# Optimization experiments

Measured on AMD Instinct MI355X. Metric: run time of the kernel, lower is better.

Reference implementation:

```python
import jax, jax.numpy as jnp
import numpy as np
import math

D_MODEL = 1024
EPS = 1e-6  # RMSNorm epsilon


def setup_inputs() -> dict:
    key = jax.random.key(0)
    ks = jax.random.split(key, 9)
    d = D_MODEL
    B, T = 4, 4096
    s = 1.0 / math.sqrt(d)
    return {
        "x": jax.random.normal(ks[0], (B, T, d), dtype=jnp.float32),
        "w_key": jax.random.normal(ks[1], (2 * d, d), dtype=jnp.float32) * s,  # Linear(d, 2d, bias=False)
        "conv_w": jax.random.normal(ks[2], (d, 1, 3), dtype=jnp.float32) * (1.0 / math.sqrt(3)),  # depthwise k=3
        "conv_b": jax.random.normal(ks[3], (d,), dtype=jnp.float32) * 0.02,
        "w1": jax.random.normal(ks[4], (2 * d, d), dtype=jnp.float32) * s,  # Linear(d, 2d)
        "b1": jax.random.normal(ks[5], (2 * d,), dtype=jnp.float32) * 0.02,
        "w2": jax.random.normal(ks[6], (d, 2 * d), dtype=jnp.float32) * (1.0 / math.sqrt(2 * d)),  # Linear(2d, d)
        "b2": jax.random.normal(ks[7], (d,), dtype=jnp.float32) * 0.02,
        "norm_w": jnp.ones((d,), dtype=jnp.float32),
    }


def parallel_lerp_scan(theta, alpha):
    # h_t = lerp(h_{t-1}, theta_t, alpha_t) = (1-alpha_t)*h_{t-1} + alpha_t*theta_t
    # Linear recurrence h_t = a_t*h_{t-1} + b_t -> log-depth associative scan.
    a = 1.0 - alpha
    b = alpha * theta

    def combine(c1, c2):
        a1, b1 = c1
        a2, b2 = c2
        return (a2 * a1, a2 * b1 + b2)

    _, h = jax.lax.associative_scan(combine, (a, b), axis=1)
    return h


def rms_norm(x, w):
    var = jnp.mean(jnp.square(x), axis=-1, keepdims=True)
    return x * jax.lax.rsqrt(var + EPS) * w


def reference(x, w_key, conv_w, conv_b, w1, b1, w2, b2, norm_w):
    d = x.shape[-1]
    res = jnp.einsum('btd,ed->bte', x, w_key)  # [B,T,2D]
    theta, alpha = res[..., :d], res[..., d:]
    h = parallel_lerp_scan(jnp.tanh(theta) * math.pi, jax.nn.sigmoid(alpha))
    h = h.astype(x.dtype)
    # causal depthwise conv: left-pad (k-1)=2 zeros along time
    h_t = jnp.transpose(h, (0, 2, 1))  # [B,D,T]
    conv = jax.lax.conv_general_dilated(
        h_t, conv_w, window_strides=(1,), padding=[(2, 0)],
        feature_group_count=d, dimension_numbers=('NCH', 'OIH', 'NCH'))
    h_bound = jnp.transpose(conv + conv_b[None, :, None], (0, 2, 1))  # [B,T,D]
    z = h + h_bound
    hid = jax.nn.silu(jnp.einsum('btd,ed->bte', z, w1) + b1)
    h_final = jnp.einsum('bte,de->btd', hid, w2) + b2
    return rms_norm(h_final, norm_w)
```

## Files before the change

### kernel.cpp

```cpp
#include <hip/hip_runtime.h>

typedef unsigned short u16;
typedef unsigned int u32;
typedef __attribute__((ext_vector_type(8))) short short8;
typedef __attribute__((ext_vector_type(4))) float f32x4;

#define T_LEN 4096
#define BATCH 4
#define M_TOT (BATCH*T_LEN)
#define NCHUNK 32
#define CLEN 128

__device__ __forceinline__ u16 f2bf(float f){
  u32 u = __builtin_bit_cast(u32, f);
  u32 r = (u + 0x7FFFu + ((u >> 16) & 1u)) >> 16;
  return (u16)r;
}
__device__ __forceinline__ float bf2f(u16 h){
  u32 u = ((u32)h) << 16; return __builtin_bit_cast(float, u);
}
__device__ __forceinline__ float sigmoid_(float v){ return 1.f/(1.f + __expf(-v)); }
__device__ __forceinline__ float tanh_pi_(float v){
  return 3.14159265358979323846f * (1.f - 2.f/(1.f + __expf(2.f*v)));
}

__global__ __launch_bounds__(256) void cvt_bf16_k(const float* __restrict__ in,
                                                  u16* __restrict__ out, int n4){
  int g = blockIdx.x*256 + threadIdx.x;
  if (g >= n4) return;
  float4 v = reinterpret_cast<const float4*>(in)[g];
  reinterpret_cast<ushort4*>(out)[g] =
      make_ushort4(f2bf(v.x), f2bf(v.y), f2bf(v.z), f2bf(v.w));
}

#define BAR() __builtin_amdgcn_s_barrier()
#define VMCNT(n) asm volatile("s_waitcnt vmcnt(" #n ")" ::: "memory")
#define PRIO1() __builtin_amdgcn_s_setprio(1)
#define PRIO0() __builtin_amdgcn_s_setprio(0)
#define SGBPIN(R) do { __builtin_amdgcn_sched_group_barrier(0x100, R, 0); \
                       __builtin_amdgcn_sched_group_barrier(0x008, 16, 0); } while(0)

#define STAGE(buf, ab, q, kt) do { \
  const u16* _s = ((ab) ? Bb : Ab) + (size_t)(q)*rowK64 + (size_t)(kt)*64; \
  __builtin_amdgcn_global_load_lds( \
    (const __attribute__((address_space(1))) void*)_s, \
    (__attribute__((address_space(3))) void*)(smem + (buf)*65536 + (ab)*32768 + (q)*8192 + stb), \
    16, 0, 0); \
} while(0)

#define LDA(buf, m, kk) (*(const short8*)(smem + (buf)*65536 + aRow + (m)*2048 + ((kk) ? csw1 : csw0)))
#define LDB(buf, n, kk) (*(const short8*)(smem + (buf)*65536 + 32768 + bRow + (n)*2048 + ((kk) ? csw1 : csw0)))

#define PFA(dst, buf, q) do { \
  dst[0] = LDA(buf, 2*(q),   0); \
  dst[1] = LDA(buf, 2*(q),   1); \
  dst[2] = LDA(buf, 2*(q)+1, 0); \
  dst[3] = LDA(buf, 2*(q)+1, 1); } while(0)

#define PFBH(d0, d1, buf, half) do { \
  d0[2*(half)]   = LDB(buf, 2*(half),   0); \
  d1[2*(half)]   = LDB(buf, 2*(half),   1); \
  d0[2*(half)+1] = LDB(buf, 2*(half)+1, 0); \
  d1[2*(half)+1] = LDB(buf, 2*(half)+1, 1); } while(0)

#define PFB(d0, d1, buf) do { PFBH(d0,d1,buf,0); PFBH(d0,d1,buf,1); } while(0)

#define MFMA_Q(q, A, B0, B1) do { _Pragma("unroll") \
  for (int n=0;n<4;n++){ \
    acc[2*(q)][n]   = __builtin_amdgcn_mfma_f32_16x16x32_bf16(A[0], B0[n], acc[2*(q)][n], 0,0,0); \
    acc[2*(q)][n]   = __builtin_amdgcn_mfma_f32_16x16x32_bf16(A[1], B1[n], acc[2*(q)][n], 0,0,0); \
    acc[2*(q)+1][n] = __builtin_amdgcn_mfma_f32_16x16x32_bf16(A[2], B0[n], acc[2*(q)+1][n], 0,0,0); \
    acc[2*(q)+1][n] = __builtin_amdgcn_mfma_f32_16x16x32_bf16(A[3], B1[n], acc[2*(q)+1][n], 0,0,0); \
  } } while(0)

template<int EPI>
__global__ __launch_bounds__(512, 2) void gemm8p(
    const u16* __restrict__ Ag, const u16* __restrict__ Bg,
    const float* __restrict__ bias, void* __restrict__ Cout,
    int M, int N, int K)
{
  extern __shared__ __attribute__((aligned(16))) char smem[];
  const int tid = threadIdx.x;
  const int wid = tid >> 6, lane = tid & 63;
  const int wr = wid >> 2, wc = wid & 3;
  const int fr = lane & 15, fq = lane >> 4;

  const int nbn = N >> 8;
  const int nwg = gridDim.x;
  const int bid = blockIdx.x;
  const int swzb = (bid & 7) * (nwg >> 3) + (bid >> 3);
  const int bm = swzb / nbn, bn = swzb - bm * nbn;

  const size_t rowK64 = (size_t)64 * K;
  const u16* Ab = Ag + ((size_t)bm*256 + (tid>>3)) * K + ((tid & 7) ^ ((tid >> 3) & 7)) * 8;
  const u16* Bb = Bg + ((size_t)bn*256 + (tid>>3)) * K + ((tid & 7) ^ ((tid >> 3) & 7)) * 8;
  const u32 stb = (u32)(wid << 10);

  const u32 aRow = (u32)(wr*128 + fr) * 128;
  const u32 bRow = (u32)(wc*64  + fr) * 128;
  const u32 csw0 = (u32)((fq*16)      ^ ((fr & 7) << 4));
  const u32 csw1 = (u32)((64 + fq*16) ^ ((fr & 7) << 4));

  f32x4 acc[8][4];
#pragma unroll
  for (int m=0;m<8;m++)
#pragma unroll
    for (int n=0;n<4;n++) acc[m][n] = f32x4{0.f,0.f,0.f,0.f};

  short8 bP0[4], bP1[4], bN0[4], bN1[4];
  short8 aP[4], aN[4];

  const int NT = K >> 6;

  STAGE(0,1,0,0); STAGE(0,1,1,0); STAGE(0,1,2,0); STAGE(0,1,3,0);
  STAGE(0,0,0,0); STAGE(0,0,1,0); STAGE(0,0,2,0); STAGE(0,0,3,0);
  STAGE(1,1,0,1); STAGE(1,1,1,1); STAGE(1,1,2,1); STAGE(1,1,3,1);
  STAGE(1,0,0,1); STAGE(1,0,2,1);
  VMCNT(6);
  BAR();
  PFB(bP0, bP1, 0);
  PFA(aP, 0, 0);

  for (int i = 0; i < (NT>>1) - 1; ++i){
    const int tt = 2*i;
    STAGE(1,0,1,tt+1); STAGE(1,0,3,tt+1);
    BAR();
    PRIO1(); PFA(aN,0,1); MFMA_Q(0, aP, bP0, bP1); PRIO0(); SGBPIN(4);
    BAR();
    STAGE(0,1,0,tt+2); STAGE(0,1,1,tt+2);
    BAR();
    PRIO1(); PFA(aP,0,2); MFMA_Q(1, aN, bP0, bP1); PRIO0(); SGBPIN(4);
    BAR();
    STAGE(0,1,2,tt+2); STAGE(0,1,3,tt+2);
    BAR();
    PRIO1(); PFA(aN,0,3); MFMA_Q(2, aP, bP0, bP1); PRIO0(); SGBPIN(4);
    BAR();
    STAGE(0,0,0,tt+2); STAGE(0,0,2,tt+2);
    BAR();
    VMCNT(6);
    PRIO1(); PFA(aP,1,0); PFBH(bN0,bN1,1,0); MFMA_Q(3, aN, bP0, bP1); PRIO0(); SGBPIN(8);
    BAR();
    STAGE(0,0,1,tt+2); STAGE(0,0,3,tt+2);
    BAR();
    PRIO1(); PFBH(bN0,bN1,1,1); PFA(aN,1,1); MFMA_Q(0, aP, bN0, bN1); PRIO0(); SGBPIN(8);
    BAR();
    STAGE(1,1,0,tt+3); STAGE(1,1,1,tt+3);
    BAR();
    PRIO1(); PFA(aP,1,2); MFMA_Q(1, aN, bN0, bN1); PRIO0(); SGBPIN(4);
    BAR();
    STAGE(1,1,2,tt+3); STAGE(1,1,3,tt+3);
    BAR();
    VMCNT(8);
    PRIO1(); PFA(aN,1,3); PFBH(bP0,bP1,0,0); MFMA_Q(2, aP, bN0, bN1); PRIO0(); SGBPIN(8);
    BAR();
    STAGE(1,0,0,tt+3); STAGE(1,0,2,tt+3);
    BAR();
    VMCNT(6);
    PRIO1(); PFA(aP,0,0); PFBH(bP0,bP1,0,1); MFMA_Q(3, aN, bN0, bN1); PRIO0(); SGBPIN(8);
    BAR();
  }
  {
    STAGE(1,0,1,NT-1); STAGE(1,0,3,NT-1);
    BAR();
    PRIO1(); PFA(aN,0,1); MFMA_Q(0, aP, bP0, bP1); PRIO0(); SGBPIN(4);
    BAR();
    BAR();
    PRIO1(); PFA(aP,0,2); MFMA_Q(1, aN, bP0, bP1); PRIO0(); SGBPIN(4);
    BAR();
    BAR();
    PRIO1(); PFA(aN,0,3); MFMA_Q(2, aP, bP0, bP1); PRIO0(); SGBPIN(4);
    BAR();
    BAR();
    VMCNT(0);
    PRIO1(); PFA(aP,1,0); PFBH(bN0,bN1,1,0); MFMA_Q(3, aN, bP0, bP1); PRIO0(); SGBPIN(8);
    BAR();
    BAR();
    PRIO1(); PFBH(bN0,bN1,1,1); PFA(aN,1,1); MFMA_Q(0, aP, bN0, bN1); PRIO0(); SGBPIN(8);
    BAR();
    BAR();
    PRIO1(); PFA(aP,1,2); MFMA_Q(1, aN, bN0, bN1); PRIO0(); SGBPIN(4);
    BAR();
    BAR();
    PRIO1(); PFA(aN,1,3); MFMA_Q(2, aP, bN0, bN1); PRIO0(); SGBPIN(4);
    BAR();
    BAR();
    PRIO1(); MFMA_Q(3, aN, bN0, bN1); PRIO0();
  }

  const int orow0 = bm*256 + wr*128;
  const int ocol0 = bn*256 + wc*64;
#pragma unroll
  for (int m=0;m<8;m++){
#pragma unroll
    for (int n=0;n<4;n++){
      const int col = ocol0 + n*16 + fr;
#pragma unroll
      for (int r=0;r<4;r++){
        const int row = orow0 + m*16 + fq*4 + r;
        float v = acc[m][n][r];
        if constexpr (EPI == 0){
          float o = (col < 1024) ? tanh_pi_(v) : sigmoid_(v);
          ((u16*)Cout)[(size_t)row*N + col] = f2bf(o);
        } else if constexpr (EPI == 1){
          v += bias[col];
          ((u16*)Cout)[(size_t)row*N + col] = f2bf(v * sigmoid_(v));
        } else {
          v += bias[col];
          ((float*)Cout)[(size_t)row*N + col] = v;
        }
      }
    }
  }
}

__global__ __launch_bounds__(256) void scan_stage1(const u16* __restrict__ res,
                                                   float* __restrict__ sA,
                                                   float* __restrict__ sB,
                                                   float* __restrict__ sA2,
                                                   float* __restrict__ sB2){
  const int c     = (blockIdx.x & 3)*256 + threadIdx.x;
  const int chunk = (blockIdx.x >> 2) & (NCHUNK-1);
  const int b     = blockIdx.x >> 7;
  const u16* p = res + ((size_t)(b*T_LEN + chunk*CLEN))*2048 + c;
  float A = 1.f, Bv = 0.f;
#pragma unroll 4
  for (int t=0;t<CLEN-1;++t){
    float th = bf2f(p[0]);
    float s  = bf2f(p[1024]);
    float a  = 1.f - s;
    A  *= a;
    Bv  = a*Bv + s*th;
    p  += 2048;
  }
  const int idx = (b*NCHUNK + chunk)*1024 + c;
  sA2[idx] = A; sB2[idx] = Bv;
  {
    float th = bf2f(p[0]);
    float s  = bf2f(p[1024]);
    float a  = 1.f - s;
    A  *= a;
    Bv  = a*Bv + s*th;
  }
  sA[idx] = A; sB[idx] = Bv;
}

__global__ __launch_bounds__(256) void scan_stage2(const float* __restrict__ sA,
                                                   const float* __restrict__ sB,
                                                   float* __restrict__ Hp){
  const int g = blockIdx.x*256 + threadIdx.x;
  const int b = g >> 10, c = g & 1023;
  float H = 0.f;
#pragma unroll
  for (int i=0;i<NCHUNK;++i){
    const int idx = (b*NCHUNK + i)*1024 + c;
    Hp[idx] = H;
    H = sA[idx]*H + sB[idx];
  }
}

__global__ __launch_bounds__(256) void scan3_conv_k(const u16* __restrict__ res,
                                                    const float* __restrict__ Hp,
                                                    const float* __restrict__ sA2,
                                                    const float* __restrict__ sB2,
                                                    const float* __restrict__ cw,
                                                    const float* __restrict__ cb,
                                                    u16* __restrict__ z){
  const int c     = (blockIdx.x & 3)*256 + threadIdx.x;
  const int chunk = (blockIdx.x >> 2) & (NCHUNK-1);
  const int b     = blockIdx.x >> 7;
  const u16* p = res + ((size_t)(b*T_LEN + chunk*CLEN))*2048 + c;
  u16*       q = z   + ((size_t)(b*T_LEN + chunk*CLEN))*1024 + c;
  const int idx = (b*NCHUNK + chunk)*1024 + c;
  float H   = Hp[idx];
  float hm1 = H;
  float hm2 = 0.f;
  if (chunk > 0){
    const int pidx = idx - 1024;
    hm2 = sA2[pidx]*Hp[pidx] + sB2[pidx];
  }
  const float w0 = cw[3*c], w1 = cw[3*c+1], w2 = cw[3*c+2], bb = cb[c];
#pragma unroll 4
  for (int t=0;t<CLEN;++t){
    float th = bf2f(p[0]);
    float s  = bf2f(p[1024]);
    H = (1.f - s)*H + s*th;
    float v = H + bb + hm2*w0 + hm1*w1 + H*w2;
    q[0] = f2bf(v);
    hm2 = hm1; hm1 = H;
    p += 2048; q += 1024;
  }
}

__global__ __launch_bounds__(256) void rmsnorm_k(float* __restrict__ io,
                                                 const float* __restrict__ w){
  const int row = blockIdx.x;
  const int tid = threadIdx.x;
  float* p = io + (size_t)row*1024;
  float4 v = reinterpret_cast<const float4*>(p)[tid];
  float ss = v.x*v.x + v.y*v.y + v.z*v.z + v.w*v.w;
#pragma unroll
  for (int o=32; o>0; o>>=1) ss += __shfl_xor(ss, o, 64);
  __shared__ float red[4];
  if ((tid & 63) == 0) red[tid >> 6] = ss;
  __syncthreads();
  float tot = red[0] + red[1] + red[2] + red[3];
  float scale = rsqrtf(tot * (1.f/1024.f) + 1e-6f);
  float4 wv = reinterpret_cast<const float4*>(w)[tid];
  float4 o;
  o.x = v.x*scale*wv.x; o.y = v.y*scale*wv.y;
  o.z = v.z*scale*wv.z; o.w = v.w*scale*wv.w;
  reinterpret_cast<float4*>(p)[tid] = o;
}

extern "C" void kernel_launch(void* const* d_in, const int* in_sizes, int n_in,
                              void* d_out, int out_size, void* d_ws, size_t ws_size,
                              hipStream_t stream) {
  const float* x      = (const float*)d_in[0];
  const float* w_key  = (const float*)d_in[1];
  const float* conv_w = (const float*)d_in[2];
  const float* conv_b = (const float*)d_in[3];
  const float* w1     = (const float*)d_in[4];
  const float* b1     = (const float*)d_in[5];
  const float* w2     = (const float*)d_in[6];
  const float* b2     = (const float*)d_in[7];
  const float* norm_w = (const float*)d_in[8];
  float* out = (float*)d_out;
  char*  ws  = (char*)d_ws;

  size_t off = 0;
  u16*   RES  = (u16*)  (ws + off); off += (size_t)M_TOT*2048*2;
  u16*   XB   = (u16*)  (ws + off); off += (size_t)M_TOT*1024*2;
  u16*   WK   = (u16*)  (ws + off); off += (size_t)2048*1024*2;
  u16*   W1B  = (u16*)  (ws + off); off += (size_t)2048*1024*2;
  u16*   W2B  = (u16*)  (ws + off); off += (size_t)1024*2048*2;
  float* SA   = (float*)(ws + off); off += (size_t)BATCH*NCHUNK*1024*4;
  float* SB   = (float*)(ws + off); off += (size_t)BATCH*NCHUNK*1024*4;
  float* SA2  = (float*)(ws + off); off += (size_t)BATCH*NCHUNK*1024*4;
  float* SB2  = (float*)(ws + off); off += (size_t)BATCH*NCHUNK*1024*4;
  float* HP   = (float*)(ws + off); off += (size_t)BATCH*NCHUNK*1024*4;
  u16* ZB  = XB;
  u16* HID = RES;

  hipFuncSetAttribute((const void*)gemm8p<0>, hipFuncAttributeMaxDynamicSharedMemorySize, 131072);
  hipFuncSetAttribute((const void*)gemm8p<1>, hipFuncAttributeMaxDynamicSharedMemorySize, 131072);
  hipFuncSetAttribute((const void*)gemm8p<2>, hipFuncAttributeMaxDynamicSharedMemorySize, 131072);

  cvt_bf16_k<<<(M_TOT*1024/4 + 255)/256, 256, 0, stream>>>(x,     XB,  M_TOT*1024/4);
  cvt_bf16_k<<<(2048*1024/4  + 255)/256, 256, 0, stream>>>(w_key, WK,  2048*1024/4);
  cvt_bf16_k<<<(2048*1024/4  + 255)/256, 256, 0, stream>>>(w1,    W1B, 2048*1024/4);
  cvt_bf16_k<<<(1024*2048/4  + 255)/256, 256, 0, stream>>>(w2,    W2B, 1024*2048/4);

  gemm8p<0><<<(M_TOT/256)*(2048/256), 512, 131072, stream>>>(XB, WK, nullptr, RES, M_TOT, 2048, 1024);

  scan_stage1<<<BATCH*NCHUNK*4, 256, 0, stream>>>(RES, SA, SB, SA2, SB2);
  scan_stage2<<<16, 256, 0, stream>>>(SA, SB, HP);
  scan3_conv_k<<<BATCH*NCHUNK*4, 256, 0, stream>>>(RES, HP, SA2, SB2, conv_w, conv_b, ZB);

  gemm8p<1><<<(M_TOT/256)*(2048/256), 512, 131072, stream>>>(ZB, W1B, b1, HID, M_TOT, 2048, 1024);

  gemm8p<2><<<(M_TOT/256)*(1024/256), 512, 131072, stream>>>(HID, W2B, b2, out, M_TOT, 1024, 2048);

  rmsnorm_k<<<M_TOT, 256, 0, stream>>>(out, norm_w);
}
```

Measured before the change: 314.5 us.

## Restructure GEMM LDS pipeline and widen scan kernels to two channels per thread

The GEMM main loop drops the register double-buffered A/B fragment prefetch. It now reads fragments for each 128x64 quadrant just before use, with explicit lgkmcnt waits and no sched_group_barrier pinning. This reduces register pressure but exposes LDS latency more. Separately, the scan uses 64 chunks of 64 steps instead of 32 of 128, and each scan thread handles two adjacent channels with ushort2/float2 accesses, so the grid keeps its size while serial length per thread halves. This halves the serial latency of each scan thread, at the cost of a longer serial stage2 across more chunks.

```diff
diff --git a/kernel.cpp b/kernel.cpp
--- a/kernel.cpp
+++ b/kernel.cpp
@@ -8,8 +8,8 @@
 #define T_LEN 4096
 #define BATCH 4
 #define M_TOT (BATCH*T_LEN)
-#define NCHUNK 32
-#define CLEN 128
+#define NCHUNK 64
+#define CLEN 64
 
 __device__ __forceinline__ u16 f2bf(float f){
   u32 u = __builtin_bit_cast(u32, f);
@@ -35,10 +35,11 @@
 
 #define BAR() __builtin_amdgcn_s_barrier()
 #define VMCNT(n) asm volatile("s_waitcnt vmcnt(" #n ")" ::: "memory")
+#define LGKM0() asm volatile("s_waitcnt lgkmcnt(0)" ::: "memory")
+#define LGKM8() asm volatile("s_waitcnt lgkmcnt(8)" ::: "memory")
+#define FEN() asm volatile("" ::: "memory")
 #define PRIO1() __builtin_amdgcn_s_setprio(1)
 #define PRIO0() __builtin_amdgcn_s_setprio(0)
-#define SGBPIN(R) do { __builtin_amdgcn_sched_group_barrier(0x100, R, 0); \
-                       __builtin_amdgcn_sched_group_barrier(0x008, 16, 0); } while(0)
 
 #define STAGE(buf, ab, q, kt) do { \
   const u16* _s = ((ab) ? Bb : Ab) + (size_t)(q)*rowK64 + (size_t)(kt)*64; \
@@ -48,30 +49,28 @@
     16, 0, 0); \
 } while(0)
 
-#define LDA(buf, m, kk) (*(const short8*)(smem + (buf)*65536 + aRow + (m)*2048 + ((kk) ? csw1 : csw0)))
-#define LDB(buf, n, kk) (*(const short8*)(smem + (buf)*65536 + 32768 + bRow + (n)*2048 + ((kk) ? csw1 : csw0)))
-
-#define PFA(dst, buf, q) do { \
-  dst[0] = LDA(buf, 2*(q),   0); \
-  dst[1] = LDA(buf, 2*(q),   1); \
-  dst[2] = LDA(buf, 2*(q)+1, 0); \
-  dst[3] = LDA(buf, 2*(q)+1, 1); } while(0)
-
-#define PFBH(d0, d1, buf, half) do { \
-  d0[2*(half)]   = LDB(buf, 2*(half),   0); \
-  d1[2*(half)]   = LDB(buf, 2*(half),   1); \
-  d0[2*(half)+1] = LDB(buf, 2*(half)+1, 0); \
-  d1[2*(half)+1] = LDB(buf, 2*(half)+1, 1); } while(0)
-
-#define PFB(d0, d1, buf) do { PFBH(d0,d1,buf,0); PFBH(d0,d1,buf,1); } while(0)
-
-#define MFMA_Q(q, A, B0, B1) do { _Pragma("unroll") \
-  for (int n=0;n<4;n++){ \
-    acc[2*(q)][n]   = __builtin_amdgcn_mfma_f32_16x16x32_bf16(A[0], B0[n], acc[2*(q)][n], 0,0,0); \
-    acc[2*(q)][n]   = __builtin_amdgcn_mfma_f32_16x16x32_bf16(A[1], B1[n], acc[2*(q)][n], 0,0,0); \
-    acc[2*(q)+1][n] = __builtin_amdgcn_mfma_f32_16x16x32_bf16(A[2], B0[n], acc[2*(q)+1][n], 0,0,0); \
-    acc[2*(q)+1][n] = __builtin_amdgcn_mfma_f32_16x16x32_bf16(A[3], B1[n], acc[2*(q)+1][n], 0,0,0); \
-  } } while(0)
+#define LDA(base, m, kk) (*(const short8*)((base) + (m)*2048 + ((kk) ? csw1 : csw0)))
+#define LDB(base, n, kk) (*(const short8*)((base) + (n)*2048 + ((kk) ? csw1 : csw0)))
+
+#define RD_A(base, h) do { _Pragma("unroll") \
+  for (int ml=0; ml<4; ml++){ \
+    aF[ml*2+0] = LDA(base, 4*(h)+ml, 0); \
+    aF[ml*2+1] = LDA(base, 4*(h)+ml, 1); } } while(0)
+
+#define RD_B(base, h) do { _Pragma("unroll") \
+  for (int nl=0; nl<2; nl++){ \
+    bF[(h)*4+nl*2+0] = LDB(base, 2*(h)+nl, 0); \
+    bF[(h)*4+nl*2+1] = LDB(base, 2*(h)+nl, 1); } } while(0)
+
+#define MFMAQ(mh, nh) do { _Pragma("unroll") \
+  for (int kk=0; kk<2; kk++) \
+  _Pragma("unroll") \
+  for (int ml=0; ml<4; ml++) \
+  _Pragma("unroll") \
+  for (int nl=0; nl<2; nl++) \
+    acc[4*(mh)+ml][2*(nh)+nl] = __builtin_amdgcn_mfma_f32_16x16x32_bf16( \
+      aF[ml*2+kk], bF[(nh)*4+nl*2+kk], acc[4*(mh)+ml][2*(nh)+nl], 0,0,0); \
+} while(0)
 
 template<int EPI>
 __global__ __launch_bounds__(512, 2) void gemm8p(
@@ -96,10 +95,12 @@
   const u16* Bb = Bg + ((size_t)bn*256 + (tid>>3)) * K + ((tid & 7) ^ ((tid >> 3) & 7)) * 8;
   const u32 stb = (u32)(wid << 10);
 
-  const u32 aRow = (u32)(wr*128 + fr) * 128;
-  const u32 bRow = (u32)(wc*64  + fr) * 128;
   const u32 csw0 = (u32)((fq*16)      ^ ((fr & 7) << 4));
   const u32 csw1 = (u32)((64 + fq*16) ^ ((fr & 7) << 4));
+  const char* aB0 = smem +         (u32)(wr*128 + fr) * 128;
+  const char* aB1 = aB0 + 65536;
+  const char* bB0 = smem + 32768 + (u32)(wc*64  + fr) * 128;
+  const char* bB1 = bB0 + 65536;
 
   f32x4 acc[8][4];
 #pragma unroll
@@ -107,84 +108,95 @@
 #pragma unroll
     for (int n=0;n<4;n++) acc[m][n] = f32x4{0.f,0.f,0.f,0.f};
 
-  short8 bP0[4], bP1[4], bN0[4], bN1[4];
-  short8 aP[4], aN[4];
+  short8 aF[8];
+  short8 bF[8];
 
   const int NT = K >> 6;
 
+  STAGE(0,0,0,0); STAGE(0,0,1,0); STAGE(0,0,2,0); STAGE(0,0,3,0);
   STAGE(0,1,0,0); STAGE(0,1,1,0); STAGE(0,1,2,0); STAGE(0,1,3,0);
-  STAGE(0,0,0,0); STAGE(0,0,1,0); STAGE(0,0,2,0); STAGE(0,0,3,0);
+  STAGE(1,0,0,1); STAGE(1,0,2,1);
   STAGE(1,1,0,1); STAGE(1,1,1,1); STAGE(1,1,2,1); STAGE(1,1,3,1);
-  STAGE(1,0,0,1); STAGE(1,0,2,1);
   VMCNT(6);
   BAR();
-  PFB(bP0, bP1, 0);
-  PFA(aP, 0, 0);
 
   for (int i = 0; i < (NT>>1) - 1; ++i){
     const int tt = 2*i;
+    RD_A(aB0,0); RD_B(bB0,0); FEN();
     STAGE(1,0,1,tt+1); STAGE(1,0,3,tt+1);
-    BAR();
-    PRIO1(); PFA(aN,0,1); MFMA_Q(0, aP, bP0, bP1); PRIO0(); SGBPIN(4);
-    BAR();
+    LGKM8();
+    BAR(); LGKM0();
+    PRIO1(); MFMAQ(0,0); PRIO0();
+    BAR();
+    RD_B(bB0,1); FEN();
+    STAGE(0,0,0,tt+2); STAGE(0,0,2,tt+2);
+    BAR(); LGKM0();
+    PRIO1(); MFMAQ(0,1); PRIO0();
+    BAR();
+    RD_A(aB0,1); FEN();
     STAGE(0,1,0,tt+2); STAGE(0,1,1,tt+2);
-    BAR();
-    PRIO1(); PFA(aP,0,2); MFMA_Q(1, aN, bP0, bP1); PRIO0(); SGBPIN(4);
+    BAR(); LGKM0();
+    PRIO1(); MFMAQ(1,0); PRIO0();
     BAR();
     STAGE(0,1,2,tt+2); STAGE(0,1,3,tt+2);
     BAR();
-    PRIO1(); PFA(aN,0,3); MFMA_Q(2, aP, bP0, bP1); PRIO0(); SGBPIN(4);
-    BAR();
-    STAGE(0,0,0,tt+2); STAGE(0,0,2,tt+2);
-    BAR();
+    PRIO1(); MFMAQ(1,1); PRIO0();
     VMCNT(6);
-    PRIO1(); PFA(aP,1,0); PFBH(bN0,bN1,1,0); MFMA_Q(3, aN, bP0, bP1); PRIO0(); SGBPIN(8);
-    BAR();
+    BAR();
+    RD_A(aB1,0); RD_B(bB1,0); FEN();
     STAGE(0,0,1,tt+2); STAGE(0,0,3,tt+2);
-    BAR();
-    PRIO1(); PFBH(bN0,bN1,1,1); PFA(aN,1,1); MFMA_Q(0, aP, bN0, bN1); PRIO0(); SGBPIN(8);
-    BAR();
+    LGKM8();
+    BAR(); LGKM0();
+    PRIO1(); MFMAQ(0,0); PRIO0();
+    BAR();
+    RD_B(bB1,1); FEN();
+    STAGE(1,0,0,tt+3); STAGE(1,0,2,tt+3);
+    BAR(); LGKM0();
+    PRIO1(); MFMAQ(0,1); PRIO0();
+    BAR();
+    RD_A(aB1,1); FEN();
     STAGE(1,1,0,tt+3); STAGE(1,1,1,tt+3);
-    BAR();
-    PRIO1(); PFA(aP,1,2); MFMA_Q(1, aN, bN0, bN1); PRIO0(); SGBPIN(4);
+    BAR(); LGKM0();
+    PRIO1(); MFMAQ(1,0); PRIO0();
     BAR();
     STAGE(1,1,2,tt+3); STAGE(1,1,3,tt+3);
     BAR();
-    VMCNT(8);
-    PRIO1(); PFA(aN,1,3); PFBH(bP0,bP1,0,0); MFMA_Q(2, aP, bN0, bN1); PRIO0(); SGBPIN(8);
-    BAR();
-    STAGE(1,0,0,tt+3); STAGE(1,0,2,tt+3);
-    BAR();
+    PRIO1(); MFMAQ(1,1); PRIO0();
     VMCNT(6);
-    PRIO1(); PFA(aP,0,0); PFBH(bP0,bP1,0,1); MFMA_Q(3, aN, bN0, bN1); PRIO0(); SGBPIN(8);
     BAR();
   }
   {
+    RD_A(aB0,0); RD_B(bB0,0); FEN();
     STAGE(1,0,1,NT-1); STAGE(1,0,3,NT-1);
-    BAR();
-    PRIO1(); PFA(aN,0,1); MFMA_Q(0, aP, bP0, bP1); PRIO0(); SGBPIN(4);
-    BAR();
-    BAR();
-    PRIO1(); PFA(aP,0,2); MFMA_Q(1, aN, bP0, bP1); PRIO0(); SGBPIN(4);
-    BAR();
-    BAR();
-    PRIO1(); PFA(aN,0,3); MFMA_Q(2, aP, bP0, bP1); PRIO0(); SGBPIN(4);
-    BAR();
-    BAR();
+    LGKM8();
+    BAR(); LGKM0();
+    PRIO1(); MFMAQ(0,0); PRIO0();
+    BAR();
+    RD_B(bB0,1); FEN();
+    BAR(); LGKM0();
+    PRIO1(); MFMAQ(0,1); PRIO0();
+    BAR();
+    RD_A(aB0,1); FEN();
+    BAR(); LGKM0();
+    PRIO1(); MFMAQ(1,0); PRIO0();
+    BAR();
+    BAR();
+    PRIO1(); MFMAQ(1,1); PRIO0();
     VMCNT(0);
-    PRIO1(); PFA(aP,1,0); PFBH(bN0,bN1,1,0); MFMA_Q(3, aN, bP0, bP1); PRIO0(); SGBPIN(8);
-    BAR();
-    BAR();
-    PRIO1(); PFBH(bN0,bN1,1,1); PFA(aN,1,1); MFMA_Q(0, aP, bN0, bN1); PRIO0(); SGBPIN(8);
-    BAR();
-    BAR();
-    PRIO1(); PFA(aP,1,2); MFMA_Q(1, aN, bN0, bN1); PRIO0(); SGBPIN(4);
-    BAR();
-    BAR();
-    PRIO1(); PFA(aN,1,3); MFMA_Q(2, aP, bN0, bN1); PRIO0(); SGBPIN(4);
-    BAR();
-    BAR();
-    PRIO1(); MFMA_Q(3, aN, bN0, bN1); PRIO0();
+    BAR();
+    RD_A(aB1,0); RD_B(bB1,0); FEN();
+    BAR(); LGKM0();
+    PRIO1(); MFMAQ(0,0); PRIO0();
+    BAR();
+    RD_B(bB1,1); FEN();
+    BAR(); LGKM0();
+    PRIO1(); MFMAQ(0,1); PRIO0();
+    BAR();
+    RD_A(aB1,1); FEN();
+    BAR(); LGKM0();
+    PRIO1(); MFMAQ(1,0); PRIO0();
+    BAR();
+    PRIO1(); MFMAQ(1,1); PRIO0();
   }
 
   const int orow0 = bm*256 + wr*128;
@@ -218,30 +230,34 @@
                                                    float* __restrict__ sB,
                                                    float* __restrict__ sA2,
                                                    float* __restrict__ sB2){
-  const int c     = (blockIdx.x & 3)*256 + threadIdx.x;
-  const int chunk = (blockIdx.x >> 2) & (NCHUNK-1);
+  const int c0    = ((blockIdx.x & 1)*256 + threadIdx.x)*2;
+  const int chunk = (blockIdx.x >> 1) & (NCHUNK-1);
   const int b     = blockIdx.x >> 7;
-  const u16* p = res + ((size_t)(b*T_LEN + chunk*CLEN))*2048 + c;
-  float A = 1.f, Bv = 0.f;
+  const u16* p = res + ((size_t)(b*T_LEN + chunk*CLEN))*2048 + c0;
+  float A0=1.f, B0v=0.f, A1=1.f, B1v=0.f;
 #pragma unroll 4
   for (int t=0;t<CLEN-1;++t){
-    float th = bf2f(p[0]);
-    float s  = bf2f(p[1024]);
-    float a  = 1.f - s;
-    A  *= a;
-    Bv  = a*Bv + s*th;
-    p  += 2048;
-  }
-  const int idx = (b*NCHUNK + chunk)*1024 + c;
-  sA2[idx] = A; sB2[idx] = Bv;
+    ushort2 th = *reinterpret_cast<const ushort2*>(p);
+    ushort2 sg = *reinterpret_cast<const ushort2*>(p+1024);
+    float s0 = bf2f(sg.x), s1 = bf2f(sg.y);
+    float a0 = 1.f - s0,   a1 = 1.f - s1;
+    A0 *= a0;  B0v = a0*B0v + s0*bf2f(th.x);
+    A1 *= a1;  B1v = a1*B1v + s1*bf2f(th.y);
+    p += 2048;
+  }
+  const int idx = (b*NCHUNK + chunk)*1024 + c0;
+  *reinterpret_cast<float2*>(&sA2[idx]) = make_float2(A0, A1);
+  *reinterpret_cast<float2*>(&sB2[idx]) = make_float2(B0v, B1v);
   {
-    float th = bf2f(p[0]);
-    float s  = bf2f(p[1024]);
-    float a  = 1.f - s;
-    A  *= a;
-    Bv  = a*Bv + s*th;
-  }
-  sA[idx] = A; sB[idx] = Bv;
+    ushort2 th = *reinterpret_cast<const ushort2*>(p);
+    ushort2 sg = *reinterpret_cast<const ushort2*>(p+1024);
+    float s0 = bf2f(sg.x), s1 = bf2f(sg.y);
+    float a0 = 1.f - s0,   a1 = 1.f - s1;
+    A0 *= a0;  B0v = a0*B0v + s0*bf2f(th.x);
+    A1 *= a1;  B1v = a1*B1v + s1*bf2f(th.y);
+  }
+  *reinterpret_cast<float2*>(&sA[idx]) = make_float2(A0, A1);
+  *reinterpret_cast<float2*>(&sB[idx]) = make_float2(B0v, B1v);
 }
 
 __global__ __launch_bounds__(256) void scan_stage2(const float* __restrict__ sA,
@@ -265,28 +281,34 @@
                                                     const float* __restrict__ cw,
                                                     const float* __restrict__ cb,
                                                     u16* __restrict__ z){
-  const int c     = (blockIdx.x & 3)*256 + threadIdx.x;
-  const int chunk = (blockIdx.x >> 2) & (NCHUNK-1);
+  const int c0    = ((blockIdx.x & 1)*256 + threadIdx.x)*2;
+  const int chunk = (blockIdx.x >> 1) & (NCHUNK-1);
   const int b     = blockIdx.x >> 7;
-  const u16* p = res + ((size_t)(b*T_LEN + chunk*CLEN))*2048 + c;
-  u16*       q = z   + ((size_t)(b*T_LEN + chunk*CLEN))*1024 + c;
-  const int idx = (b*NCHUNK + chunk)*1024 + c;
-  float H   = Hp[idx];
-  float hm1 = H;
-  float hm2 = 0.f;
+  const u16* p = res + ((size_t)(b*T_LEN + chunk*CLEN))*2048 + c0;
+  u16*       q = z   + ((size_t)(b*T_LEN + chunk*CLEN))*1024 + c0;
+  const int idx = (b*NCHUNK + chunk)*1024 + c0;
+  float H0 = Hp[idx], H1 = Hp[idx+1];
+  float hm1_0 = H0, hm1_1 = H1;
+  float hm2_0 = 0.f, hm2_1 = 0.f;
   if (chunk > 0){
     const int pidx = idx - 1024;
-    hm2 = sA2[pidx]*Hp[pidx] + sB2[pidx];
-  }
-  const float w0 = cw[3*c], w1 = cw[3*c+1], w2 = cw[3*c+2], bb = cb[c];
+    hm2_0 = sA2[pidx]*Hp[pidx] + sB2[pidx];
+    hm2_1 = sA2[pidx+1]*Hp[pidx+1] + sB2[pidx+1];
+  }
+  const float w0_0 = cw[3*c0],   w1_0 = cw[3*c0+1], w2_0 = cw[3*c0+2], bb0 = cb[c0];
+  const float w0_1 = cw[3*c0+3], w1_1 = cw[3*c0+4], w2_1 = cw[3*c0+5], bb1 = cb[c0+1];
 #pragma unroll 4
   for (int t=0;t<CLEN;++t){
-    float th = bf2f(p[0]);
-    float s  = bf2f(p[1024]);
-    H = (1.f - s)*H + s*th;
-    float v = H + bb + hm2*w0 + hm1*w1 + H*w2;
-    q[0] = f2bf(v);
-    hm2 = hm1; hm1 = H;
+    ushort2 th = *reinterpret_cast<const ushort2*>(p);
+    ushort2 sg = *reinterpret_cast<const ushort2*>(p+1024);
+    float s0 = bf2f(sg.x), s1 = bf2f(sg.y);
+    H0 = (1.f - s0)*H0 + s0*bf2f(th.x);
+    H1 = (1.f - s1)*H1 + s1*bf2f(th.y);
+    float v0 = H0 + bb0 + hm2_0*w0_0 + hm1_0*w1_0 + H0*w2_0;
+    float v1 = H1 + bb1 + hm2_1*w0_1 + hm1_1*w1_1 + H1*w2_1;
+    *reinterpret_cast<ushort2*>(q) = make_ushort2(f2bf(v0), f2bf(v1));
+    hm2_0 = hm1_0; hm1_0 = H0;
+    hm2_1 = hm1_1; hm1_1 = H1;
     p += 2048; q += 1024;
   }
 }
@@ -352,9 +374,9 @@
 
   gemm8p<0><<<(M_TOT/256)*(2048/256), 512, 131072, stream>>>(XB, WK, nullptr, RES, M_TOT, 2048, 1024);
 
-  scan_stage1<<<BATCH*NCHUNK*4, 256, 0, stream>>>(RES, SA, SB, SA2, SB2);
+  scan_stage1<<<BATCH*NCHUNK*2, 256, 0, stream>>>(RES, SA, SB, SA2, SB2);
   scan_stage2<<<16, 256, 0, stream>>>(SA, SB, HP);
-  scan3_conv_k<<<BATCH*NCHUNK*4, 256, 0, stream>>>(RES, HP, SA2, SB2, conv_w, conv_b, ZB);
+  scan3_conv_k<<<BATCH*NCHUNK*2, 256, 0, stream>>>(RES, HP, SA2, SB2, conv_w, conv_b, ZB);
 
   gemm8p<1><<<(M_TOT/256)*(2048/256), 512, 131072, stream>>>(ZB, W1B, b1, HID, M_TOT, 2048, 1024);
 
```

After: 308.3 us. 1.02x faster.
